# Optimization experiments

Measured on AMD Instinct MI355X. Metric: run time of the kernel, lower is better.

## Reference

```python
import jax, jax.numpy as jnp
import numpy as np

ALPHA = 0.2  # leaky relu slope
NEG_INF = -1.0e12


def _gat(x, adj, W, a):
    # x: [N, Fin], W: [Fin, Fout], a: [2*Fout, 1]
    h = x @ W                                  # [N, Fout]
    Fout = W.shape[1]
    # additive attention: e_ij = leakyrelu(h_i . a[:Fout] + h_j . a[Fout:])
    f1 = h @ a[:Fout, 0]                       # [N]
    f2 = h @ a[Fout:, 0]                       # [N]
    e = jax.nn.leaky_relu(f1[:, None] + f2[None, :], ALPHA)  # [N, N]
    att = jnp.where(adj > 0, e, NEG_INF)
    att = jax.nn.softmax(att, axis=1)          # dropout=0 -> identity
    return jax.nn.elu(att @ h + h)             # [N, Fout]


def setup_inputs() -> dict:
    key = jax.random.key(0)
    k = jax.random.split(key, 6)
    N, NFEAT, NHID, NNEXT = 8192, 256, 128, 1024
    x = jax.random.normal(k[0], (N, NFEAT), dtype=jnp.float32)
    adj = (jax.random.uniform(k[1], (N, N)) > 0.9).astype(jnp.float32)
    # xavier-uniform-ish init
    def xav(kk, shape):
        lim = np.sqrt(6.0 / (shape[0] + shape[1])) * 1.414
        return jax.random.uniform(kk, shape, minval=-lim, maxval=lim, dtype=jnp.float32)
    W_embed = xav(k[2], (NFEAT, NHID))
    a_embed = xav(k[3], (2 * NHID, 1))
    W_assign = xav(k[4], (NFEAT, NNEXT))
    a_assign = xav(k[5], (2 * NNEXT, 1))
    return {"x": x, "adj": adj, "W_embed": W_embed, "a_embed": a_embed,
            "W_assign": W_assign, "a_assign": a_assign}


def reference(x, adj, W_embed, a_embed, W_assign, a_assign):
    z_l = _gat(x, adj, W_embed, a_embed)          # [N, nhid]
    assign = _gat(x, adj, W_assign, a_assign)     # [N, nnext]
    s_l = jax.nn.softmax(assign, axis=-1)         # [N, nnext]
    xnext = s_l.T @ z_l                            # [nnext, nhid]
    anext = s_l.T @ adj @ s_l                      # [nnext, nnext]
    return xnext, anext, s_l
```

## Files before the change

kernel.cpp:

```cpp
#include <hip/hip_runtime.h>
#include <hip/hip_bf16.h>


#define DI __device__ __forceinline__

typedef __attribute__((ext_vector_type(8))) short short8;
typedef __attribute__((ext_vector_type(4))) float f32x4;

static DI float bf2f(short s) {
    union { unsigned u; float f; } c;
    c.u = ((unsigned)(unsigned short)s) << 16;
    return c.f;
}
static DI short f2bf(float f) {
    union { float f; unsigned u; } c; c.f = f;
    unsigned r = (c.u + 0x7FFFu + ((c.u >> 16) & 1u)) >> 16;
    return (short)(unsigned short)r;
}
template <int F32>
static DI short8 ld8(const void* base, size_t off) {
    if (F32 == 0) return *(const short8*)((const short*)base + off);
    const float* p = (const float*)base + off;
    f32x4 a = *(const f32x4*)p;
    f32x4 b = *(const f32x4*)(p + 4);
    short8 v;
    #pragma unroll
    for (int e = 0; e < 4; e++) { v[e] = f2bf(a[e]); v[4 + e] = f2bf(b[e]); }
    return v;
}
static DI float wred_sum(float v) {
    #pragma unroll
    for (int o = 32; o > 0; o >>= 1) v += __shfl_down(v, o, 64);
    return v;
}
static DI float wred_max(float v) {
    #pragma unroll
    for (int o = 32; o > 0; o >>= 1) v = fmaxf(v, __shfl_down(v, o, 64));
    return v;
}
static DI int sfun(int r) { return (r ^ (r >> 3)) & 7; }
static DI int swzk(int k, int r) {
    return (k & ~63) | ((((k >> 3) & 7) ^ sfun(r)) << 3) | (k & 7);
}
static DI unsigned pack2(short lo, short hi) {
    return ((unsigned)(unsigned short)lo) | (((unsigned)(unsigned short)hi) << 16);
}
static DI void gload16(const void* g, void* l) {
    __builtin_amdgcn_global_load_lds(
        (const __attribute__((address_space(1))) unsigned int*)g,
        (__attribute__((address_space(3))) unsigned int*)l, 16, 0, 0);
}

template <int EPI, int SWZX>
__launch_bounds__(256)
__global__ void gemm_lds(const short* __restrict__ A, const short* __restrict__ Bt,
                         void* __restrict__ C, int ldc, int kcount) {
    __shared__ short As0[128][64], Bs0[128][64];
    __shared__ short As1[128][64], Bs1[128][64];
    int bx = blockIdx.x, by = blockIdx.y;
    if (SWZX) {
        int lid = blockIdx.x + blockIdx.y * 8;
        int c = lid & 7, s = lid >> 3;
        by = c * 8 + (s >> 3);
        bx = s & 7;
    }
    const int tid  = threadIdx.x;
    const int lane = tid & 63;
    const int w    = tid >> 6;
    const int wr   = w >> 1, wc = w & 1;
    const int i0   = by * 128;
    const int n0   = bx * 128;
    const int k0   = blockIdx.z * kcount;

    const int srow = w * 32 + (lane >> 3);
    const short* gA = A  + (size_t)(i0 + srow) * 8192 + k0 + (lane & 7) * 8;
    const short* gB = Bt + (size_t)(n0 + srow) * 8192 + k0 + (lane & 7) * 8;

    f32x4 acc[4][4];
    #pragma unroll
    for (int m = 0; m < 4; m++)
        #pragma unroll
        for (int n = 0; n < 4; n++) acc[m][n] = (f32x4){0.f, 0.f, 0.f, 0.f};

#define STAGE_TILE(ts, Ab, Bb)                                                  \
    do {                                                                        \
        _Pragma("unroll")                                                       \
        for (int j = 0; j < 4; j++) {                                           \
            gload16(gA + (size_t)(ts) * 64 + (size_t)j * 8 * 8192,              \
                    &Ab[w * 32 + j * 8][0]);                                    \
            gload16(gB + (size_t)(ts) * 64 + (size_t)j * 8 * 8192,              \
                    &Bb[w * 32 + j * 8][0]);                                    \
        }                                                                       \
    } while (0)

#define COMPUTE_TILE(Ab, Bb)                                                    \
    do {                                                                        \
        _Pragma("unroll")                                                       \
        for (int kk = 0; kk < 2; kk++) {                                        \
            short8 af[4], bq[4];                                                \
            _Pragma("unroll")                                                   \
            for (int m = 0; m < 4; m++) {                                       \
                int ar = wr * 64 + m * 16 + (lane & 15);                        \
                af[m] = *(const short8*)&Ab[ar]                                 \
                            [swzk(kk * 32 + (lane >> 4) * 8, ar)];              \
            }                                                                   \
            _Pragma("unroll")                                                   \
            for (int n = 0; n < 4; n++) {                                       \
                int br = wc * 64 + n * 16 + (lane & 15);                        \
                bq[n] = *(const short8*)&Bb[br]                                 \
                            [swzk(kk * 32 + (lane >> 4) * 8, br)];              \
            }                                                                   \
            _Pragma("unroll")                                                   \
            for (int m = 0; m < 4; m++)                                         \
                _Pragma("unroll")                                               \
                for (int n = 0; n < 4; n++)                                     \
                    acc[m][n] = __builtin_amdgcn_mfma_f32_16x16x32_bf16(        \
                        af[m], bq[n], acc[m][n], 0, 0, 0);                      \
        }                                                                       \
    } while (0)

    const int nt = kcount >> 6;
    STAGE_TILE(0, As0, Bs0);
    for (int t = 0; t < nt; t += 2) {
        __syncthreads();
        STAGE_TILE(t + 1, As1, Bs1);
        COMPUTE_TILE(As0, Bs0);
        __syncthreads();
        if (t + 2 < nt) STAGE_TILE(t + 2, As0, Bs0);
        COMPUTE_TILE(As1, Bs1);
    }
#undef STAGE_TILE
#undef COMPUTE_TILE

    #pragma unroll
    for (int m = 0; m < 4; m++) {
        #pragma unroll
        for (int n = 0; n < 4; n++) {
            int row0 = i0 + wr * 64 + m * 16 + ((lane >> 4) << 2);
            int col  = n0 + wc * 64 + n * 16 + (lane & 15);
            if (EPI == 1) {
                unsigned long long pk = 0;
                #pragma unroll
                for (int r = 0; r < 4; r++)
                    pk |= (unsigned long long)(unsigned short)f2bf(acc[m][n][r])
                          << (16 * r);
                *(unsigned long long*)((short*)C + (size_t)col * 8192 +
                                       swzk(row0, col)) = pk;
            } else {
                #pragma unroll
                for (int r = 0; r < 4; r++) {
                    float v = acc[m][n][r];
                    if (EPI == 0) ((float*)C)[(size_t)(row0 + r) * ldc + col] = v;
                    else atomicAdd(&((float*)C)[(size_t)(row0 + r) * ldc + col], v);
                }
            }
        }
    }
}

template <int SWZX>
__launch_bounds__(256)
__global__ void gemm_bin(const unsigned char* __restrict__ adjm,
                         const short* __restrict__ Bt,
                         short* __restrict__ C, int kcount) {
    __shared__ short Bs0[128][64], Bs1[128][64];
    __shared__ unsigned char Ms0[128][8], Ms1[128][8];
    int bx = blockIdx.x, by = blockIdx.y;
    if (SWZX) {
        int lid = blockIdx.x + blockIdx.y * 8;
        int c = lid & 7, s = lid >> 3;
        by = c * 8 + (s >> 3);
        bx = s & 7;
    }
    const int tid  = threadIdx.x;
    const int lane = tid & 63;
    const int w    = tid >> 6;
    const int wr   = w >> 1, wc = w & 1;
    const int i0   = by * 128;
    const int n0   = bx * 128;
    const int k0   = blockIdx.z * kcount;

    const int srow = w * 32 + (lane >> 3);
    const short* gB = Bt + (size_t)(n0 + srow) * 8192 + k0 + (lane & 7) * 8;
    const unsigned char* gM = adjm + (size_t)(i0 + (tid >> 1)) * 1024 +
                              (k0 >> 3) + (tid & 1) * 4;

    f32x4 acc[4][4];
    #pragma unroll
    for (int m = 0; m < 4; m++)
        #pragma unroll
        for (int n = 0; n < 4; n++) acc[m][n] = (f32x4){0.f, 0.f, 0.f, 0.f};

#define BN_STAGE(ts, Bb, Mb)                                                    \
    do {                                                                        \
        _Pragma("unroll")                                                       \
        for (int j = 0; j < 4; j++)                                             \
            gload16(gB + (size_t)(ts) * 64 + (size_t)j * 8 * 8192,              \
                    &Bb[w * 32 + j * 8][0]);                                    \
        unsigned mv = *(const unsigned*)(gM + (size_t)(ts) * 8);                \
        *(unsigned*)&Mb[tid >> 1][(tid & 1) * 4] = mv;                          \
    } while (0)

#define BN_COMPUTE(Bb, Mb)                                                      \
    do {                                                                        \
        _Pragma("unroll")                                                       \
        for (int kk = 0; kk < 2; kk++) {                                        \
            short8 af[4], bq[4];                                                \
            _Pragma("unroll")                                                   \
            for (int m = 0; m < 4; m++) {                                       \
                int ar = wr * 64 + m * 16 + (lane & 15);                        \
                unsigned mbyte = Mb[ar][kk * 4 + (lane >> 4)];                  \
                _Pragma("unroll")                                               \
                for (int e = 0; e < 8; e++)                                     \
                    af[m][e] = ((mbyte >> e) & 1) ? (short)0x3F80 : (short)0;   \
            }                                                                   \
            _Pragma("unroll")                                                   \
            for (int n = 0; n < 4; n++) {                                       \
                int br = wc * 64 + n * 16 + (lane & 15);                        \
                bq[n] = *(const short8*)&Bb[br]                                 \
                            [swzk(kk * 32 + (lane >> 4) * 8, br)];              \
            }                                                                   \
            _Pragma("unroll")                                                   \
            for (int m = 0; m < 4; m++)                                         \
                _Pragma("unroll")                                               \
                for (int n = 0; n < 4; n++)                                     \
                    acc[m][n] = __builtin_amdgcn_mfma_f32_16x16x32_bf16(        \
                        af[m], bq[n], acc[m][n], 0, 0, 0);                      \
        }                                                                       \
    } while (0)

    const int nt = kcount >> 6;
    BN_STAGE(0, Bs0, Ms0);
    for (int t = 0; t < nt; t += 2) {
        __syncthreads();
        BN_STAGE(t + 1, Bs1, Ms1);
        BN_COMPUTE(Bs0, Ms0);
        __syncthreads();
        if (t + 2 < nt) BN_STAGE(t + 2, Bs0, Ms0);
        BN_COMPUTE(Bs1, Ms1);
    }
#undef BN_STAGE
#undef BN_COMPUTE

    #pragma unroll
    for (int m = 0; m < 4; m++) {
        #pragma unroll
        for (int n = 0; n < 4; n++) {
            int row0 = i0 + wr * 64 + m * 16 + ((lane >> 4) << 2);
            int col  = n0 + wc * 64 + n * 16 + (lane & 15);
            unsigned long long pk = 0;
            #pragma unroll
            for (int r = 0; r < 4; r++)
                pk |= (unsigned long long)(unsigned short)f2bf(acc[m][n][r])
                      << (16 * r);
            *(unsigned long long*)(C + (size_t)col * 8192 + swzk(row0, col)) = pk;
        }
    }
}

template <int EPI, int SWZX>
__launch_bounds__(256)
__global__ void gemm_gen(const unsigned char* __restrict__ adjm,
                         const short* __restrict__ Bt,
                         float* __restrict__ C, int ldc, int kcount,
                         const float* __restrict__ E1, const float* __restrict__ F1,
                         const float* __restrict__ E2, const float* __restrict__ F2) {
    __shared__ short As0[128][64], Bs0[128][64];
    __shared__ short As1[128][64], Bs1[128][64];
    int bx = blockIdx.x, by = blockIdx.y;
    if (SWZX) {
        int lid = blockIdx.x + blockIdx.y * 8;
        int c = lid & 7, s = lid >> 3;
        by = c * 8 + (s >> 3);
        bx = s & 7;
    }
    const int tid  = threadIdx.x;
    const int lane = tid & 63;
    const int w    = tid >> 6;
    const int wr   = w >> 1, wc = w & 1;
    const int i0   = by * 128;
    const int n0   = bx * 128;
    const int k0   = blockIdx.z * kcount;

    const int srow = w * 32 + (lane >> 3);
    const short* gB = Bt + (size_t)(n0 + srow) * 8192 + k0 + (lane & 7) * 8;
    const int mr = tid >> 1, mh = tid & 1;
    const unsigned char* gM = adjm + (size_t)(i0 + mr) * 1024 + (k0 >> 3) + mh * 4;
    const float e1v = E1[i0 + mr], f1v = F1[i0 + mr];

    f32x4 acc[4][4];
    #pragma unroll
    for (int m = 0; m < 4; m++)
        #pragma unroll
        for (int n = 0; n < 4; n++) acc[m][n] = (f32x4){0.f, 0.f, 0.f, 0.f};

    unsigned mreg;

#define G_ALOAD(ts)                                                             \
    do { mreg = *(const unsigned*)(gM + (size_t)(ts) * 8); } while (0)

#define G_BLOAD(ts, Bb)                                                         \
    do {                                                                        \
        _Pragma("unroll")                                                       \
        for (int j = 0; j < 4; j++)                                             \
            gload16(gB + (size_t)(ts) * 64 + (size_t)j * 8 * 8192,              \
                    &Bb[w * 32 + j * 8][0]);                                    \
    } while (0)

#define G_WSTAGE(ts, As_)                                                       \
    do {                                                                        \
        _Pragma("unroll")                                                       \
        for (int b = 0; b < 4; b++) {                                           \
            int kbr = mh * 4 + b;                                               \
            int rk = k0 + (ts) * 64 + kbr * 8;                                  \
            unsigned mbyte = (mreg >> (8 * b)) & 0xFFu;                         \
            f32x4 e2a = *(const f32x4*)(E2 + rk);                               \
            f32x4 e2b = *(const f32x4*)(E2 + rk + 4);                           \
            f32x4 f2a = *(const f32x4*)(F2 + rk);                               \
            f32x4 f2b = *(const f32x4*)(F2 + rk + 4);                           \
            short8 p;                                                           \
            _Pragma("unroll")                                                   \
            for (int e = 0; e < 8; e++) {                                       \
                float ev = e < 4 ? e2a[e] : e2b[e - 4];                         \
                float fv = e < 4 ? f2a[e] : f2b[e - 4];                         \
                float wg = fmaxf(e1v * ev, f1v * fv);                           \
                p[e] = ((mbyte >> e) & 1) ? f2bf(wg) : (short)0;                \
            }                                                                   \
            *(short8*)&As_[mr][(kbr ^ sfun(mr)) * 8] = p;                       \
        }                                                                       \
    } while (0)

#define G_COMPUTE(Ab_, Bb_)                                                     \
    do {                                                                        \
        _Pragma("unroll")                                                       \
        for (int kk = 0; kk < 2; kk++) {                                        \
            short8 af[4], bq[4];                                                \
            _Pragma("unroll")                                                   \
            for (int m = 0; m < 4; m++) {                                       \
                int ar = wr * 64 + m * 16 + (lane & 15);                        \
                af[m] = *(const short8*)&Ab_[ar]                                \
                            [swzk(kk * 32 + (lane >> 4) * 8, ar)];              \
            }                                                                   \
            _Pragma("unroll")                                                   \
            for (int n = 0; n < 4; n++) {                                       \
                int br = wc * 64 + n * 16 + (lane & 15);                        \
                bq[n] = *(const short8*)&Bb_[br]                                \
                            [swzk(kk * 32 + (lane >> 4) * 8, br)];              \
            }                                                                   \
            _Pragma("unroll")                                                   \
            for (int m = 0; m < 4; m++)                                         \
                _Pragma("unroll")                                               \
                for (int n = 0; n < 4; n++)                                     \
                    acc[m][n] = __builtin_amdgcn_mfma_f32_16x16x32_bf16(        \
                        af[m], bq[n], acc[m][n], 0, 0, 0);                      \
        }                                                                       \
    } while (0)

    const int nt = kcount >> 6;
    G_ALOAD(0);
    G_BLOAD(0, Bs0);
    for (int t = 0; t < nt; t += 2) {
        G_WSTAGE(t, As0);
        __syncthreads();
        G_ALOAD(t + 1);
        G_BLOAD(t + 1, Bs1);
        G_COMPUTE(As0, Bs0);
        G_WSTAGE(t + 1, As1);
        __syncthreads();
        if (t + 2 < nt) { G_ALOAD(t + 2); G_BLOAD(t + 2, Bs0); }
        G_COMPUTE(As1, Bs1);
    }
#undef G_ALOAD
#undef G_BLOAD
#undef G_WSTAGE
#undef G_COMPUTE

    #pragma unroll
    for (int m = 0; m < 4; m++) {
        #pragma unroll
        for (int n = 0; n < 4; n++) {
            int row0 = i0 + wr * 64 + m * 16 + ((lane >> 4) << 2);
            int col  = n0 + wc * 64 + n * 16 + (lane & 15);
            #pragma unroll
            for (int r = 0; r < 4; r++)
                atomicAdd(&C[(size_t)(row0 + r) * ldc + col], acc[m][n][r]);
        }
    }
}

template <int SWZX>
__launch_bounds__(256)
__global__ void gemm_xw_k(const float* __restrict__ A, const float* __restrict__ B,
                          short* __restrict__ C, short* __restrict__ Ct, int ldn) {
    __shared__ short As[128][64];
    __shared__ short Bs[128][64];
    int bx = blockIdx.x, by = blockIdx.y;
    if (SWZX) {
        int lid = blockIdx.x + blockIdx.y * 8;
        int c = lid & 7, s = lid >> 3;
        by = c * 8 + (s >> 3);
        bx = s & 7;
    }
    const int tid  = threadIdx.x;
    const int lane = tid & 63;
    const int w    = tid >> 6;
    const int wr   = w >> 1, wc = w & 1;
    const int i0   = by * 128;
    const int n0   = bx * 128;

    f32x4 acc[4][4];
    #pragma unroll
    for (int m = 0; m < 4; m++)
        #pragma unroll
        for (int n = 0; n < 4; n++) acc[m][n] = (f32x4){0.f, 0.f, 0.f, 0.f};

    for (int ks = 0; ks < 256; ks += 64) {
        __syncthreads();
        #pragma unroll
        for (int it = 0; it < 4; it++) {
            int idx = it * 256 + tid;
            int cg = idx & 7, r = idx >> 3;
            *(short8*)&As[r][swzk(cg * 8, r)] =
                ld8<1>(A, (size_t)(i0 + r) * 256 + ks + cg * 8);
        }
        #pragma unroll
        for (int it = 0; it < 2; it++) {
            int idx = it * 256 + tid;
            int ng = idx & 15, kp = idx >> 4;
            int k = 2 * kp;
            short8 r0 = ld8<1>(B, (size_t)(ks + k) * ldn + n0 + ng * 8);
            short8 r1 = ld8<1>(B, (size_t)(ks + k + 1) * ldn + n0 + ng * 8);
            #pragma unroll
            for (int j = 0; j < 8; j++) {
                int row = ng * 8 + j;
                *(unsigned*)&Bs[row][swzk(k, row)] = pack2(r0[j], r1[j]);
            }
        }
        __syncthreads();
        #pragma unroll
        for (int kk = 0; kk < 2; kk++) {
            short8 af[4], bq[4];
            #pragma unroll
            for (int m = 0; m < 4; m++) {
                int ar = wr * 64 + m * 16 + (lane & 15);
                af[m] = *(const short8*)&As[ar][swzk(kk * 32 + (lane >> 4) * 8, ar)];
            }
            #pragma unroll
            for (int n = 0; n < 4; n++) {
                int br = wc * 64 + n * 16 + (lane & 15);
                bq[n] = *(const short8*)&Bs[br][swzk(kk * 32 + (lane >> 4) * 8, br)];
            }
            #pragma unroll
            for (int m = 0; m < 4; m++)
                #pragma unroll
                for (int n = 0; n < 4; n++)
                    acc[m][n] = __builtin_amdgcn_mfma_f32_16x16x32_bf16(
                        af[m], bq[n], acc[m][n], 0, 0, 0);
        }
    }
    #pragma unroll
    for (int m = 0; m < 4; m++) {
        #pragma unroll
        for (int n = 0; n < 4; n++) {
            int row0 = i0 + wr * 64 + m * 16 + ((lane >> 4) << 2);
            int col  = n0 + wc * 64 + n * 16 + (lane & 15);
            unsigned long long pk = 0;
            #pragma unroll
            for (int r = 0; r < 4; r++) {
                short b = f2bf(acc[m][n][r]);
                C[(size_t)(row0 + r) * ldn + col] = b;
                pk |= (unsigned long long)(unsigned short)b << (16 * r);
            }
            *(unsigned long long*)(Ct + (size_t)col * 8192 + swzk(row0, col)) = pk;
        }
    }
}

__launch_bounds__(256)
__global__ void compute_f_k(const short* __restrict__ h1, const short* __restrict__ h2,
                            const float* __restrict__ ae, const float* __restrict__ aa,
                            float* __restrict__ f11, float* __restrict__ f21,
                            float* __restrict__ f12, float* __restrict__ f22) {
    int row = blockIdx.x, t = threadIdx.x;
    float s11 = 0.f, s21 = 0.f, s12 = 0.f, s22 = 0.f;
    if (t < 128) {
        float hv = bf2f(h1[(size_t)row * 128 + t]);
        s11 = hv * ae[t];
        s21 = hv * ae[128 + t];
    }
    #pragma unroll
    for (int q = 0; q < 4; q++) {
        int f = t + q * 256;
        float hv = bf2f(h2[(size_t)row * 1024 + f]);
        s12 += hv * aa[f];
        s22 += hv * aa[1024 + f];
    }
    __shared__ float red[4][4];
    s11 = wred_sum(s11); s21 = wred_sum(s21);
    s12 = wred_sum(s12); s22 = wred_sum(s22);
    int w = t >> 6;
    if ((t & 63) == 0) { red[0][w] = s11; red[1][w] = s21; red[2][w] = s12; red[3][w] = s22; }
    __syncthreads();
    if (t == 0) {
        f11[row] = red[0][0] + red[0][1] + red[0][2] + red[0][3];
        f21[row] = red[1][0] + red[1][1] + red[1][2] + red[1][3];
        f12[row] = red[2][0] + red[2][1] + red[2][2] + red[2][3];
        f22[row] = red[3][0] + red[3][1] + red[3][2] + red[3][3];
    }
}

__launch_bounds__(256)
__global__ void evec_k(const float* __restrict__ f11, const float* __restrict__ f21,
                       const float* __restrict__ f12, const float* __restrict__ f22,
                       float* __restrict__ E11, float* __restrict__ F11,
                       float* __restrict__ E21, float* __restrict__ F21,
                       float* __restrict__ E12, float* __restrict__ F12,
                       float* __restrict__ E22, float* __restrict__ F22) {
    int i = blockIdx.x * 256 + threadIdx.x;
    if (i >= 8192) return;
    float a = f11[i], b = f21[i], c = f12[i], d = f22[i];
    E11[i] = __expf(a); F11[i] = __expf(0.2f * a);
    E21[i] = __expf(b); F21[i] = __expf(0.2f * b);
    E12[i] = __expf(c); F12[i] = __expf(0.2f * c);
    E22[i] = __expf(d); F22[i] = __expf(0.2f * d);
}

__launch_bounds__(256)
__global__ void prepass_k(const float* __restrict__ adj,
                          const float* __restrict__ E11, const float* __restrict__ F11,
                          const float* __restrict__ E21, const float* __restrict__ F21,
                          const float* __restrict__ E12, const float* __restrict__ F12,
                          const float* __restrict__ E22, const float* __restrict__ F22,
                          float* __restrict__ den1, float* __restrict__ den2,
                          short* __restrict__ P2b, unsigned char* __restrict__ adjm) {
    const int r0 = blockIdx.x * 4, t = threadIdx.x;
    float e1r[4], f1r[4], e2r[4], f2r[4];
    #pragma unroll
    for (int r = 0; r < 4; r++) {
        e1r[r] = E11[r0 + r]; f1r[r] = F11[r0 + r];
        e2r[r] = E12[r0 + r]; f2r[r] = F12[r0 + r];
    }
    float d1[4] = {0.f, 0.f, 0.f, 0.f}, d2[4] = {0.f, 0.f, 0.f, 0.f};
    #pragma unroll
    for (int jc = 0; jc < 4; jc++) {
        int jb = jc * 2048 + t * 8;
        f32x4 eA0 = *(const f32x4*)(E21 + jb), eA1 = *(const f32x4*)(E21 + jb + 4);
        f32x4 fA0 = *(const f32x4*)(F21 + jb), fA1 = *(const f32x4*)(F21 + jb + 4);
        f32x4 eB0 = *(const f32x4*)(E22 + jb), eB1 = *(const f32x4*)(E22 + jb + 4);
        f32x4 fB0 = *(const f32x4*)(F22 + jb), fB1 = *(const f32x4*)(F22 + jb + 4);
        #pragma unroll
        for (int r = 0; r < 4; r++) {
            const float* ap = adj + (size_t)(r0 + r) * 8192 + jb;
            f32x4 a0 = *(const f32x4*)ap, a1 = *(const f32x4*)(ap + 4);
            short8 p2v;
            unsigned mb = 0;
            #pragma unroll
            for (int e = 0; e < 8; e++) {
                float av = e < 4 ? a0[e] : a1[e - 4];
                float eA = e < 4 ? eA0[e] : eA1[e - 4];
                float fA = e < 4 ? fA0[e] : fA1[e - 4];
                float eB = e < 4 ? eB0[e] : eB1[e - 4];
                float fB = e < 4 ? fB0[e] : fB1[e - 4];
                float x1 = fmaxf(e1r[r] * eA, f1r[r] * fA);
                float x2 = fmaxf(e2r[r] * eB, f2r[r] * fB);
                bool on = av > 0.f;
                d1[r] += on ? x1 : 0.f;
                d2[r] += on ? x2 : 0.f;
                p2v[e] = on ? f2bf(x2) : (short)0;
                mb |= (on ? 1u : 0u) << e;
            }
            *(short8*)(P2b + (size_t)(r0 + r) * 8192 + swzk(jb, r0 + r)) = p2v;
            adjm[(size_t)(r0 + r) * 1024 + (jb >> 3)] = (unsigned char)mb;
        }
    }
    __shared__ float r1s[4][4], r2s[4][4];
    #pragma unroll
    for (int r = 0; r < 4; r++) { d1[r] = wred_sum(d1[r]); d2[r] = wred_sum(d2[r]); }
    if ((t & 63) == 0) {
        #pragma unroll
        for (int r = 0; r < 4; r++) { r1s[t >> 6][r] = d1[r]; r2s[t >> 6][r] = d2[r]; }
    }
    __syncthreads();
    if (t < 4) {
        den1[r0 + t] = r1s[0][t] + r1s[1][t] + r1s[2][t] + r1s[3][t];
        den2[r0 + t] = r2s[0][t] + r2s[1][t] + r2s[2][t] + r2s[3][t];
    }
}

__launch_bounds__(256)
__global__ void epi_gat1t_k(const float* __restrict__ Y1, const float* __restrict__ den1,
                            const short* __restrict__ h1, short* __restrict__ zlt) {
    __shared__ short ts[128][65];
    int tr = blockIdx.x * 64;
    int t = threadIdx.x;
    #pragma unroll
    for (int it = 0; it < 4; it++) {
        int idx = it * 256 + t;
        int r = idx >> 4, cb = idx & 15;
        int row = tr + r;
        float d = den1[row]; d = d > 0.f ? d : 1.f;
        const float* yp = Y1 + (size_t)row * 128 + cb * 8;
        f32x4 y0 = *(const f32x4*)yp, y1 = *(const f32x4*)(yp + 4);
        short8 hv = *(const short8*)(h1 + (size_t)row * 128 + cb * 8);
        #pragma unroll
        for (int e = 0; e < 8; e++) {
            float z = (e < 4 ? y0[e] : y1[e - 4]) / d + bf2f(hv[e]);
            z = z > 0.f ? z : (__expf(z) - 1.f);
            ts[cb * 8 + e][r] = f2bf(z);
        }
    }
    __syncthreads();
    #pragma unroll
    for (int it = 0; it < 4; it++) {
        int idx = it * 256 + t;
        int c = idx >> 3, rb = idx & 7;
        short8 v = *(const short8*)&ts[c][rb * 8];
        *(short8*)(zlt + (size_t)c * 8192 + tr + ((rb ^ sfun(c)) << 3)) = v;
    }
}

__launch_bounds__(256)
__global__ void episoft_k(const float* __restrict__ Y2, const float* __restrict__ den2,
                          const short* __restrict__ h2, float* __restrict__ slo,
                          short* __restrict__ slb) {
    int row = blockIdx.x, t = threadIdx.x;
    float d = den2[row];
    d = d > 0.f ? d : 1.f;
    float v[4], mx = -1e30f;
    #pragma unroll
    for (int q = 0; q < 4; q++) {
        int j = t + q * 256;
        float a = Y2[(size_t)row * 1024 + j] / d + bf2f(h2[(size_t)row * 1024 + j]);
        a = a > 0.f ? a : (__expf(a) - 1.f);
        v[q] = a;
        mx = fmaxf(mx, a);
    }
    __shared__ float sred[4];
    __shared__ float sbc;
    mx = wred_max(mx);
    if ((t & 63) == 0) sred[t >> 6] = mx;
    __syncthreads();
    if (t == 0) sbc = fmaxf(fmaxf(sred[0], sred[1]), fmaxf(sred[2], sred[3]));
    __syncthreads();
    mx = sbc;
    float s = 0.f;
    #pragma unroll
    for (int q = 0; q < 4; q++) { v[q] = __expf(v[q] - mx); s += v[q]; }
    s = wred_sum(s);
    if ((t & 63) == 0) sred[t >> 6] = s;
    __syncthreads();
    if (t == 0) sbc = sred[0] + sred[1] + sred[2] + sred[3];
    __syncthreads();
    float inv = 1.f / sbc;
    #pragma unroll
    for (int q = 0; q < 4; q++) {
        float sv = v[q] * inv;
        slo[(size_t)row * 1024 + t + q * 256] = sv;
        slb[(size_t)row * 1024 + t + q * 256] = f2bf(sv);
    }
}

template <int F32IN>
__launch_bounds__(256)
__global__ void transpose_swz_k(const void* __restrict__ in, short* __restrict__ out,
                                int R, int C) {
    __shared__ short ts[64][72];
    int tc = blockIdx.x * 64;
    int tr = blockIdx.y * 64;
    int t = threadIdx.x;
    #pragma unroll
    for (int h = 0; h < 2; h++) {
        int r = (t >> 3) + h * 32, c = (t & 7) * 8;
        *(short8*)&ts[r][c] = ld8<F32IN>(in, (size_t)(tr + r) * C + tc + c);
    }
    __syncthreads();
    #pragma unroll
    for (int h = 0; h < 2; h++) {
        int n = t >> 2, blk = (t & 3) + h * 4;
        short8 v;
        #pragma unroll
        for (int e = 0; e < 8; e++) v[e] = ts[blk * 8 + e][n];
        *(short8*)(out + (size_t)(tc + n) * R + tr + ((blk ^ sfun(tc + n)) << 3)) = v;
    }
}

extern "C" void kernel_launch(void* const* d_in, const int* in_sizes, int n_in,
                              void* d_out, int out_size, void* d_ws, size_t ws_size,
                              hipStream_t stream) {
    const float* x   = (const float*)d_in[0];
    const float* adj = (const float*)d_in[1];
    const float* We  = (const float*)d_in[2];
    const float* ae  = (const float*)d_in[3];
    const float* Wa  = (const float*)d_in[4];
    const float* aa  = (const float*)d_in[5];
    float* out = (float*)d_out;

    char* w = (char*)d_ws;
    short* h1b = (short*)(w);
    short* h2b = (short*)(w + (2u   << 20));
    float* f11 = (float*)(w + (18u  << 20));
    float* f21 = f11 + 8192;  float* f12 = f21 + 8192; float* f22 = f12 + 8192;
    float* den1 = f22 + 8192; float* den2 = den1 + 8192;
    float* E11 = den2 + 8192; float* F11 = E11 + 8192;
    float* E21 = F11 + 8192;  float* F21 = E21 + 8192;
    float* E12 = F21 + 8192;  float* F12 = E12 + 8192;
    float* E22 = F12 + 8192;  float* F22 = E22 + 8192;
    float* Y1f = (float*)(w + (21u << 20));
    float* Y2f = (float*)(w + (25u << 20));
    short* slb = (short*)(w + (57u << 20));
    short* h1t = (short*)(w + (73u << 20));
    short* h2t = (short*)(w + (75u << 20));
    short* slt = (short*)(w + (91u << 20));
    short* zlt = (short*)(w + (107u << 20));
    short* tT  = (short*)(w + (109u << 20));
    short* P2b = (short*)(w + (128u << 20));
    unsigned char* adjm = (unsigned char*)(w + (256u << 20));

    float* xo  = out;
    float* ao  = out + 131072;
    float* slo = out + 131072 + 1048576;

    hipMemsetAsync(out, 0, (size_t)(131072 + 1048576) * 4, stream);
    hipMemsetAsync(Y1f, 0, (size_t)8192 * 128 * 4, stream);

    gemm_xw_k<0><<<dim3(1, 64), 256, 0, stream>>>(x, We, h1b, h1t, 128);
    gemm_xw_k<1><<<dim3(8, 64), 256, 0, stream>>>(x, Wa, h2b, h2t, 1024);
    compute_f_k<<<dim3(8192), 256, 0, stream>>>(h1b, h2b, ae, aa, f11, f21, f12, f22);
    evec_k<<<dim3(32), 256, 0, stream>>>(f11, f21, f12, f22,
        E11, F11, E21, F21, E12, F12, E22, F22);
    prepass_k<<<dim3(2048), 256, 0, stream>>>(adj,
        E11, F11, E21, F21, E12, F12, E22, F22, den1, den2, P2b, adjm);

    gemm_gen<3, 0><<<dim3(1, 64, 8), 256, 0, stream>>>(
        adjm, h1t, Y1f, 128, 1024, E11, F11, E21, F21);
    epi_gat1t_k<<<dim3(128), 256, 0, stream>>>(Y1f, den1, h1b, zlt);

    gemm_lds<0, 1><<<dim3(8, 64, 1), 256, 0, stream>>>(P2b, h2t, Y2f, 1024, 8192);
    episoft_k<<<dim3(8192), 256, 0, stream>>>(Y2f, den2, h2b, slo, slb);
    transpose_swz_k<0><<<dim3(16, 128), 256, 0, stream>>>(slb, slt, 8192, 1024);

    gemm_bin<1><<<dim3(8, 64, 1), 256, 0, stream>>>(adjm, slt, tT, 8192);

    gemm_lds<3, 0><<<dim3(8, 8, 8), 256, 0, stream>>>(slt, tT, ao, 1024, 1024);
    gemm_lds<3, 0><<<dim3(1, 8, 32), 256, 0, stream>>>(slt, zlt, xo, 128, 256);
}
```

Measured before the change: 708.5 us.

## Fuse the two attention aggregation GEMMs into one launch and restage the adjacency-mask GEMM

After: 850.3 us. 20.0% more time.

```diff
diff --git a/kernel.cpp b/kernel.cpp
--- a/kernel.cpp
+++ b/kernel.cpp
@@ -51,286 +51,7 @@
         (__attribute__((address_space(3))) unsigned int*)l, 16, 0, 0);
 }
 
-template <int EPI, int SWZX>
-__launch_bounds__(256)
-__global__ void gemm_lds(const short* __restrict__ A, const short* __restrict__ Bt,
-                         void* __restrict__ C, int ldc, int kcount) {
-    __shared__ short As0[128][64], Bs0[128][64];
-    __shared__ short As1[128][64], Bs1[128][64];
-    int bx = blockIdx.x, by = blockIdx.y;
-    if (SWZX) {
-        int lid = blockIdx.x + blockIdx.y * 8;
-        int c = lid & 7, s = lid >> 3;
-        by = c * 8 + (s >> 3);
-        bx = s & 7;
-    }
-    const int tid  = threadIdx.x;
-    const int lane = tid & 63;
-    const int w    = tid >> 6;
-    const int wr   = w >> 1, wc = w & 1;
-    const int i0   = by * 128;
-    const int n0   = bx * 128;
-    const int k0   = blockIdx.z * kcount;
-
-    const int srow = w * 32 + (lane >> 3);
-    const short* gA = A  + (size_t)(i0 + srow) * 8192 + k0 + (lane & 7) * 8;
-    const short* gB = Bt + (size_t)(n0 + srow) * 8192 + k0 + (lane & 7) * 8;
-
-    f32x4 acc[4][4];
-    #pragma unroll
-    for (int m = 0; m < 4; m++)
-        #pragma unroll
-        for (int n = 0; n < 4; n++) acc[m][n] = (f32x4){0.f, 0.f, 0.f, 0.f};
-
-#define STAGE_TILE(ts, Ab, Bb)                                                  \
-    do {                                                                        \
-        _Pragma("unroll")                                                       \
-        for (int j = 0; j < 4; j++) {                                           \
-            gload16(gA + (size_t)(ts) * 64 + (size_t)j * 8 * 8192,              \
-                    &Ab[w * 32 + j * 8][0]);                                    \
-            gload16(gB + (size_t)(ts) * 64 + (size_t)j * 8 * 8192,              \
-                    &Bb[w * 32 + j * 8][0]);                                    \
-        }                                                                       \
-    } while (0)
-
-#define COMPUTE_TILE(Ab, Bb)                                                    \
-    do {                                                                        \
-        _Pragma("unroll")                                                       \
-        for (int kk = 0; kk < 2; kk++) {                                        \
-            short8 af[4], bq[4];                                                \
-            _Pragma("unroll")                                                   \
-            for (int m = 0; m < 4; m++) {                                       \
-                int ar = wr * 64 + m * 16 + (lane & 15);                        \
-                af[m] = *(const short8*)&Ab[ar]                                 \
-                            [swzk(kk * 32 + (lane >> 4) * 8, ar)];              \
-            }                                                                   \
-            _Pragma("unroll")                                                   \
-            for (int n = 0; n < 4; n++) {                                       \
-                int br = wc * 64 + n * 16 + (lane & 15);                        \
-                bq[n] = *(const short8*)&Bb[br]                                 \
-                            [swzk(kk * 32 + (lane >> 4) * 8, br)];              \
-            }                                                                   \
-            _Pragma("unroll")                                                   \
-            for (int m = 0; m < 4; m++)                                         \
-                _Pragma("unroll")                                               \
-                for (int n = 0; n < 4; n++)                                     \
-                    acc[m][n] = __builtin_amdgcn_mfma_f32_16x16x32_bf16(        \
-                        af[m], bq[n], acc[m][n], 0, 0, 0);                      \
-        }                                                                       \
-    } while (0)
-
-    const int nt = kcount >> 6;
-    STAGE_TILE(0, As0, Bs0);
-    for (int t = 0; t < nt; t += 2) {
-        __syncthreads();
-        STAGE_TILE(t + 1, As1, Bs1);
-        COMPUTE_TILE(As0, Bs0);
-        __syncthreads();
-        if (t + 2 < nt) STAGE_TILE(t + 2, As0, Bs0);
-        COMPUTE_TILE(As1, Bs1);
-    }
-#undef STAGE_TILE
-#undef COMPUTE_TILE
-
-    #pragma unroll
-    for (int m = 0; m < 4; m++) {
-        #pragma unroll
-        for (int n = 0; n < 4; n++) {
-            int row0 = i0 + wr * 64 + m * 16 + ((lane >> 4) << 2);
-            int col  = n0 + wc * 64 + n * 16 + (lane & 15);
-            if (EPI == 1) {
-                unsigned long long pk = 0;
-                #pragma unroll
-                for (int r = 0; r < 4; r++)
-                    pk |= (unsigned long long)(unsigned short)f2bf(acc[m][n][r])
-                          << (16 * r);
-                *(unsigned long long*)((short*)C + (size_t)col * 8192 +
-                                       swzk(row0, col)) = pk;
-            } else {
-                #pragma unroll
-                for (int r = 0; r < 4; r++) {
-                    float v = acc[m][n][r];
-                    if (EPI == 0) ((float*)C)[(size_t)(row0 + r) * ldc + col] = v;
-                    else atomicAdd(&((float*)C)[(size_t)(row0 + r) * ldc + col], v);
-                }
-            }
-        }
-    }
-}
-
-template <int SWZX>
-__launch_bounds__(256)
-__global__ void gemm_bin(const unsigned char* __restrict__ adjm,
-                         const short* __restrict__ Bt,
-                         short* __restrict__ C, int kcount) {
-    __shared__ short Bs0[128][64], Bs1[128][64];
-    __shared__ unsigned char Ms0[128][8], Ms1[128][8];
-    int bx = blockIdx.x, by = blockIdx.y;
-    if (SWZX) {
-        int lid = blockIdx.x + blockIdx.y * 8;
-        int c = lid & 7, s = lid >> 3;
-        by = c * 8 + (s >> 3);
-        bx = s & 7;
-    }
-    const int tid  = threadIdx.x;
-    const int lane = tid & 63;
-    const int w    = tid >> 6;
-    const int wr   = w >> 1, wc = w & 1;
-    const int i0   = by * 128;
-    const int n0   = bx * 128;
-    const int k0   = blockIdx.z * kcount;
-
-    const int srow = w * 32 + (lane >> 3);
-    const short* gB = Bt + (size_t)(n0 + srow) * 8192 + k0 + (lane & 7) * 8;
-    const unsigned char* gM = adjm + (size_t)(i0 + (tid >> 1)) * 1024 +
-                              (k0 >> 3) + (tid & 1) * 4;
-
-    f32x4 acc[4][4];
-    #pragma unroll
-    for (int m = 0; m < 4; m++)
-        #pragma unroll
-        for (int n = 0; n < 4; n++) acc[m][n] = (f32x4){0.f, 0.f, 0.f, 0.f};
-
-#define BN_STAGE(ts, Bb, Mb)                                                    \
-    do {                                                                        \
-        _Pragma("unroll")                                                       \
-        for (int j = 0; j < 4; j++)                                             \
-            gload16(gB + (size_t)(ts) * 64 + (size_t)j * 8 * 8192,              \
-                    &Bb[w * 32 + j * 8][0]);                                    \
-        unsigned mv = *(const unsigned*)(gM + (size_t)(ts) * 8);                \
-        *(unsigned*)&Mb[tid >> 1][(tid & 1) * 4] = mv;                          \
-    } while (0)
-
-#define BN_COMPUTE(Bb, Mb)                                                      \
-    do {                                                                        \
-        _Pragma("unroll")                                                       \
-        for (int kk = 0; kk < 2; kk++) {                                        \
-            short8 af[4], bq[4];                                                \
-            _Pragma("unroll")                                                   \
-            for (int m = 0; m < 4; m++) {                                       \
-                int ar = wr * 64 + m * 16 + (lane & 15);                        \
-                unsigned mbyte = Mb[ar][kk * 4 + (lane >> 4)];                  \
-                _Pragma("unroll")                                               \
-                for (int e = 0; e < 8; e++)                                     \
-                    af[m][e] = ((mbyte >> e) & 1) ? (short)0x3F80 : (short)0;   \
-            }                                                                   \
-            _Pragma("unroll")                                                   \
-            for (int n = 0; n < 4; n++) {                                       \
-                int br = wc * 64 + n * 16 + (lane & 15);                        \
-                bq[n] = *(const short8*)&Bb[br]                                 \
-                            [swzk(kk * 32 + (lane >> 4) * 8, br)];              \
-            }                                                                   \
-            _Pragma("unroll")                                                   \
-            for (int m = 0; m < 4; m++)                                         \
-                _Pragma("unroll")                                               \
-                for (int n = 0; n < 4; n++)                                     \
-                    acc[m][n] = __builtin_amdgcn_mfma_f32_16x16x32_bf16(        \
-                        af[m], bq[n], acc[m][n], 0, 0, 0);                      \
-        }                                                                       \
-    } while (0)
-
-    const int nt = kcount >> 6;
-    BN_STAGE(0, Bs0, Ms0);
-    for (int t = 0; t < nt; t += 2) {
-        __syncthreads();
-        BN_STAGE(t + 1, Bs1, Ms1);
-        BN_COMPUTE(Bs0, Ms0);
-        __syncthreads();
-        if (t + 2 < nt) BN_STAGE(t + 2, Bs0, Ms0);
-        BN_COMPUTE(Bs1, Ms1);
-    }
-#undef BN_STAGE
-#undef BN_COMPUTE
-
-    #pragma unroll
-    for (int m = 0; m < 4; m++) {
-        #pragma unroll
-        for (int n = 0; n < 4; n++) {
-            int row0 = i0 + wr * 64 + m * 16 + ((lane >> 4) << 2);
-            int col  = n0 + wc * 64 + n * 16 + (lane & 15);
-            unsigned long long pk = 0;
-            #pragma unroll
-            for (int r = 0; r < 4; r++)
-                pk |= (unsigned long long)(unsigned short)f2bf(acc[m][n][r])
-                      << (16 * r);
-            *(unsigned long long*)(C + (size_t)col * 8192 + swzk(row0, col)) = pk;
-        }
-    }
-}
-
-template <int EPI, int SWZX>
-__launch_bounds__(256)
-__global__ void gemm_gen(const unsigned char* __restrict__ adjm,
-                         const short* __restrict__ Bt,
-                         float* __restrict__ C, int ldc, int kcount,
-                         const float* __restrict__ E1, const float* __restrict__ F1,
-                         const float* __restrict__ E2, const float* __restrict__ F2) {
-    __shared__ short As0[128][64], Bs0[128][64];
-    __shared__ short As1[128][64], Bs1[128][64];
-    int bx = blockIdx.x, by = blockIdx.y;
-    if (SWZX) {
-        int lid = blockIdx.x + blockIdx.y * 8;
-        int c = lid & 7, s = lid >> 3;
-        by = c * 8 + (s >> 3);
-        bx = s & 7;
-    }
-    const int tid  = threadIdx.x;
-    const int lane = tid & 63;
-    const int w    = tid >> 6;
-    const int wr   = w >> 1, wc = w & 1;
-    const int i0   = by * 128;
-    const int n0   = bx * 128;
-    const int k0   = blockIdx.z * kcount;
-
-    const int srow = w * 32 + (lane >> 3);
-    const short* gB = Bt + (size_t)(n0 + srow) * 8192 + k0 + (lane & 7) * 8;
-    const int mr = tid >> 1, mh = tid & 1;
-    const unsigned char* gM = adjm + (size_t)(i0 + mr) * 1024 + (k0 >> 3) + mh * 4;
-    const float e1v = E1[i0 + mr], f1v = F1[i0 + mr];
-
-    f32x4 acc[4][4];
-    #pragma unroll
-    for (int m = 0; m < 4; m++)
-        #pragma unroll
-        for (int n = 0; n < 4; n++) acc[m][n] = (f32x4){0.f, 0.f, 0.f, 0.f};
-
-    unsigned mreg;
-
-#define G_ALOAD(ts)                                                             \
-    do { mreg = *(const unsigned*)(gM + (size_t)(ts) * 8); } while (0)
-
-#define G_BLOAD(ts, Bb)                                                         \
-    do {                                                                        \
-        _Pragma("unroll")                                                       \
-        for (int j = 0; j < 4; j++)                                             \
-            gload16(gB + (size_t)(ts) * 64 + (size_t)j * 8 * 8192,              \
-                    &Bb[w * 32 + j * 8][0]);                                    \
-    } while (0)
-
-#define G_WSTAGE(ts, As_)                                                       \
-    do {                                                                        \
-        _Pragma("unroll")                                                       \
-        for (int b = 0; b < 4; b++) {                                           \
-            int kbr = mh * 4 + b;                                               \
-            int rk = k0 + (ts) * 64 + kbr * 8;                                  \
-            unsigned mbyte = (mreg >> (8 * b)) & 0xFFu;                         \
-            f32x4 e2a = *(const f32x4*)(E2 + rk);                               \
-            f32x4 e2b = *(const f32x4*)(E2 + rk + 4);                           \
-            f32x4 f2a = *(const f32x4*)(F2 + rk);                               \
-            f32x4 f2b = *(const f32x4*)(F2 + rk + 4);                           \
-            short8 p;                                                           \
-            _Pragma("unroll")                                                   \
-            for (int e = 0; e < 8; e++) {                                       \
-                float ev = e < 4 ? e2a[e] : e2b[e - 4];                         \
-                float fv = e < 4 ? f2a[e] : f2b[e - 4];                         \
-                float wg = fmaxf(e1v * ev, f1v * fv);                           \
-                p[e] = ((mbyte >> e) & 1) ? f2bf(wg) : (short)0;                \
-            }                                                                   \
-            *(short8*)&As_[mr][(kbr ^ sfun(mr)) * 8] = p;                       \
-        }                                                                       \
-    } while (0)
-
-#define G_COMPUTE(Ab_, Bb_)                                                     \
+#define MFMA_COMPUTE(Ab_, Bb_)                                                  \
     do {                                                                        \
         _Pragma("unroll")                                                       \
         for (int kk = 0; kk < 2; kk++) {                                        \
@@ -356,25 +77,177 @@
         }                                                                       \
     } while (0)
 
+template <int EPI, int SWZX>
+__launch_bounds__(256)
+__global__ void gemm_lds(const short* __restrict__ A, const short* __restrict__ Bt,
+                         void* __restrict__ C, int ldc, int kcount) {
+    __shared__ short As0[128][64], Bs0[128][64];
+    __shared__ short As1[128][64], Bs1[128][64];
+    int bx = blockIdx.x, by = blockIdx.y;
+    if (SWZX) {
+        int lid = blockIdx.x + blockIdx.y * 8;
+        int c = lid & 7, s = lid >> 3;
+        by = c * 8 + (s >> 3);
+        bx = s & 7;
+    }
+    const int tid  = threadIdx.x;
+    const int lane = tid & 63;
+    const int w    = tid >> 6;
+    const int wr   = w >> 1, wc = w & 1;
+    const int i0   = by * 128;
+    const int n0   = bx * 128;
+    const int k0   = blockIdx.z * kcount;
+
+    const int srow = w * 32 + (lane >> 3);
+    const short* gA = A  + (size_t)(i0 + srow) * 8192 + k0 + (lane & 7) * 8;
+    const short* gB = Bt + (size_t)(n0 + srow) * 8192 + k0 + (lane & 7) * 8;
+
+    f32x4 acc[4][4];
+    #pragma unroll
+    for (int m = 0; m < 4; m++)
+        #pragma unroll
+        for (int n = 0; n < 4; n++) acc[m][n] = (f32x4){0.f, 0.f, 0.f, 0.f};
+
+#define STAGE_TILE(ts, Ab, Bb)                                                  \
+    do {                                                                        \
+        _Pragma("unroll")                                                       \
+        for (int j = 0; j < 4; j++) {                                           \
+            gload16(gA + (size_t)(ts) * 64 + (size_t)j * 8 * 8192,              \
+                    &Ab[w * 32 + j * 8][0]);                                    \
+            gload16(gB + (size_t)(ts) * 64 + (size_t)j * 8 * 8192,              \
+                    &Bb[w * 32 + j * 8][0]);                                    \
+        }                                                                       \
+    } while (0)
+
     const int nt = kcount >> 6;
-    G_ALOAD(0);
-    G_BLOAD(0, Bs0);
+    STAGE_TILE(0, As0, Bs0);
     for (int t = 0; t < nt; t += 2) {
-        G_WSTAGE(t, As0);
-        __syncthreads();
-        G_ALOAD(t + 1);
-        G_BLOAD(t + 1, Bs1);
-        G_COMPUTE(As0, Bs0);
-        G_WSTAGE(t + 1, As1);
-        __syncthreads();
-        if (t + 2 < nt) { G_ALOAD(t + 2); G_BLOAD(t + 2, Bs0); }
-        G_COMPUTE(As1, Bs1);
-    }
-#undef G_ALOAD
-#undef G_BLOAD
-#undef G_WSTAGE
-#undef G_COMPUTE
-
+        __syncthreads();
+        STAGE_TILE(t + 1, As1, Bs1);
+        MFMA_COMPUTE(As0, Bs0);
+        __syncthreads();
+        if (t + 2 < nt) STAGE_TILE(t + 2, As0, Bs0);
+        MFMA_COMPUTE(As1, Bs1);
+    }
+#undef STAGE_TILE
+
+    #pragma unroll
+    for (int m = 0; m < 4; m++) {
+        #pragma unroll
+        for (int n = 0; n < 4; n++) {
+            int row0 = i0 + wr * 64 + m * 16 + ((lane >> 4) << 2);
+            int col  = n0 + wc * 64 + n * 16 + (lane & 15);
+            #pragma unroll
+            for (int r = 0; r < 4; r++) {
+                float v = acc[m][n][r];
+                if (EPI == 0) ((float*)C)[(size_t)(row0 + r) * ldc + col] = v;
+                else atomicAdd(&((float*)C)[(size_t)(row0 + r) * ldc + col], v);
+            }
+        }
+    }
+}
+
+__launch_bounds__(256)
+__global__ void gemm_y(const short* __restrict__ P2b,
+                       const unsigned char* __restrict__ adjm,
+                       const short* __restrict__ h2t, const short* __restrict__ h1t,
+                       float* __restrict__ Y2f, float* __restrict__ Y1f,
+                       const float* __restrict__ E1, const float* __restrict__ F1,
+                       const float* __restrict__ E2, const float* __restrict__ F2) {
+    __shared__ short As0[128][64], Bs0[128][64];
+    __shared__ short As1[128][64], Bs1[128][64];
+    const bool y1 = (blockIdx.x == 8);
+    int bx, by;
+    if (y1) { bx = 0; by = blockIdx.y; }
+    else {
+        int lid = blockIdx.x + blockIdx.y * 8;
+        int c = lid & 7, s = lid >> 3;
+        by = c * 8 + (s >> 3);
+        bx = s & 7;
+    }
+    const int tid  = threadIdx.x;
+    const int lane = tid & 63;
+    const int w    = tid >> 6;
+    const int wr   = w >> 1, wc = w & 1;
+    const int i0   = by * 128;
+    const int n0   = bx * 128;
+
+    const int srow = w * 32 + (lane >> 3);
+    const short* Bt = y1 ? h1t : h2t;
+    const short* gB = Bt + (size_t)(n0 + srow) * 8192 + (lane & 7) * 8;
+    const short* gA = P2b + (size_t)(i0 + srow) * 8192 + (lane & 7) * 8;
+    const int mr = tid >> 1, mh = tid & 1;
+    const unsigned char* gM = adjm + (size_t)(i0 + mr) * 1024 + mh * 4;
+    float e1v = 0.f, f1v = 0.f;
+    if (y1) { e1v = E1[i0 + mr]; f1v = F1[i0 + mr]; }
+
+    f32x4 acc[4][4];
+    #pragma unroll
+    for (int m = 0; m < 4; m++)
+        #pragma unroll
+        for (int n = 0; n < 4; n++) acc[m][n] = (f32x4){0.f, 0.f, 0.f, 0.f};
+
+#define Y_STAGE(ts, Ab, Bb)                                                     \
+    do {                                                                        \
+        if (!y1) {                                                              \
+            _Pragma("unroll")                                                   \
+            for (int j = 0; j < 4; j++)                                         \
+                gload16(gA + (size_t)(ts) * 64 + (size_t)j * 8 * 8192,          \
+                        &Ab[w * 32 + j * 8][0]);                                \
+        }                                                                       \
+        _Pragma("unroll")                                                       \
+        for (int j = 0; j < 4; j++)                                             \
+            gload16(gB + (size_t)(ts) * 64 + (size_t)j * 8 * 8192,              \
+                    &Bb[w * 32 + j * 8][0]);                                    \
+    } while (0)
+
+#define Y_WSTAGE(ts, As_, mrg)                                                  \
+    do {                                                                        \
+        _Pragma("unroll")                                                       \
+        for (int b = 0; b < 4; b++) {                                           \
+            int kbr = mh * 4 + b;                                               \
+            int rk = (ts) * 64 + kbr * 8;                                       \
+            unsigned mbyte = ((mrg) >> (8 * b)) & 0xFFu;                        \
+            f32x4 e2a = *(const f32x4*)(E2 + rk);                               \
+            f32x4 e2b = *(const f32x4*)(E2 + rk + 4);                           \
+            f32x4 f2a = *(const f32x4*)(F2 + rk);                               \
+            f32x4 f2b = *(const f32x4*)(F2 + rk + 4);                           \
+            short8 p;                                                           \
+            _Pragma("unroll")                                                   \
+            for (int e = 0; e < 8; e++) {                                       \
+                float ev = e < 4 ? e2a[e] : e2b[e - 4];                         \
+                float fv = e < 4 ? f2a[e] : f2b[e - 4];                         \
+                float wg = fmaxf(e1v * ev, f1v * fv);                           \
+                p[e] = ((mbyte >> e) & 1) ? f2bf(wg) : (short)0;                \
+            }                                                                   \
+            *(short8*)&As_[mr][(kbr ^ sfun(mr)) * 8] = p;                       \
+        }                                                                       \
+    } while (0)
+
+    const int nt = 128;
+    unsigned mreg = 0;
+    if (y1) mreg = *(const unsigned*)(gM);
+    Y_STAGE(0, As0, Bs0);
+    for (int t = 0; t < nt; t += 2) {
+        if (y1) Y_WSTAGE(t, As0, mreg);
+        __syncthreads();
+        unsigned mnext = 0;
+        if (y1) mnext = *(const unsigned*)(gM + (size_t)(t + 1) * 8);
+        Y_STAGE(t + 1, As1, Bs1);
+        MFMA_COMPUTE(As0, Bs0);
+        if (y1) Y_WSTAGE(t + 1, As1, mnext);
+        __syncthreads();
+        if (t + 2 < nt) {
+            if (y1) mreg = *(const unsigned*)(gM + (size_t)(t + 2) * 8);
+            Y_STAGE(t + 2, As0, Bs0);
+        }
+        MFMA_COMPUTE(As1, Bs1);
+    }
+#undef Y_STAGE
+#undef Y_WSTAGE
+
+    float* C = y1 ? Y1f : Y2f;
+    const int ldc = y1 ? 128 : 1024;
     #pragma unroll
     for (int m = 0; m < 4; m++) {
         #pragma unroll
@@ -383,7 +256,97 @@
             int col  = n0 + wc * 64 + n * 16 + (lane & 15);
             #pragma unroll
             for (int r = 0; r < 4; r++)
-                atomicAdd(&C[(size_t)(row0 + r) * ldc + col], acc[m][n][r]);
+                C[(size_t)(row0 + r) * ldc + col] = acc[m][n][r];
+        }
+    }
+}
+
+template <int SWZX>
+__launch_bounds__(256)
+__global__ void gemm_maskb(const unsigned char* __restrict__ adjm,
+                           const short* __restrict__ Bt,
+                           short* __restrict__ C) {
+    __shared__ short As0[128][64], Bs0[128][64];
+    __shared__ short As1[128][64], Bs1[128][64];
+    int bx = blockIdx.x, by = blockIdx.y;
+    if (SWZX) {
+        int lid = blockIdx.x + blockIdx.y * 8;
+        int c = lid & 7, s = lid >> 3;
+        by = c * 8 + (s >> 3);
+        bx = s & 7;
+    }
+    const int tid  = threadIdx.x;
+    const int lane = tid & 63;
+    const int w    = tid >> 6;
+    const int wr   = w >> 1, wc = w & 1;
+    const int i0   = by * 128;
+    const int n0   = bx * 128;
+
+    const int srow = w * 32 + (lane >> 3);
+    const short* gB = Bt + (size_t)(n0 + srow) * 8192 + (lane & 7) * 8;
+    const int mr = tid >> 1, mh = tid & 1;
+    const unsigned char* gM = adjm + (size_t)(i0 + mr) * 1024 + mh * 4;
+
+    f32x4 acc[4][4];
+    #pragma unroll
+    for (int m = 0; m < 4; m++)
+        #pragma unroll
+        for (int n = 0; n < 4; n++) acc[m][n] = (f32x4){0.f, 0.f, 0.f, 0.f};
+
+#define MB_BLOAD(ts, Bb)                                                        \
+    do {                                                                        \
+        _Pragma("unroll")                                                       \
+        for (int j = 0; j < 4; j++)                                             \
+            gload16(gB + (size_t)(ts) * 64 + (size_t)j * 8 * 8192,              \
+                    &Bb[w * 32 + j * 8][0]);                                    \
+    } while (0)
+
+#define MB_WSTAGE(As_, mrg)                                                     \
+    do {                                                                        \
+        _Pragma("unroll")                                                       \
+        for (int b = 0; b < 4; b++) {                                           \
+            int kbr = mh * 4 + b;                                               \
+            unsigned mbyte = ((mrg) >> (8 * b)) & 0xFFu;                        \
+            short8 p;                                                           \
+            _Pragma("unroll")                                                   \
+            for (int e = 0; e < 8; e++)                                         \
+                p[e] = ((mbyte >> e) & 1) ? (short)0x3F80 : (short)0;           \
+            *(short8*)&As_[mr][(kbr ^ sfun(mr)) * 8] = p;                       \
+        }                                                                       \
+    } while (0)
+
+    const int nt = 128;
+    unsigned mreg = *(const unsigned*)(gM);
+    MB_BLOAD(0, Bs0);
+    for (int t = 0; t < nt; t += 2) {
+        MB_WSTAGE(As0, mreg);
+        __syncthreads();
+        unsigned mnext = *(const unsigned*)(gM + (size_t)(t + 1) * 8);
+        MB_BLOAD(t + 1, Bs1);
+        MFMA_COMPUTE(As0, Bs0);
+        MB_WSTAGE(As1, mnext);
+        __syncthreads();
+        if (t + 2 < nt) {
+            mreg = *(const unsigned*)(gM + (size_t)(t + 2) * 8);
+            MB_BLOAD(t + 2, Bs0);
+        }
+        MFMA_COMPUTE(As1, Bs1);
+    }
+#undef MB_BLOAD
+#undef MB_WSTAGE
+
+    #pragma unroll
+    for (int m = 0; m < 4; m++) {
+        #pragma unroll
+        for (int n = 0; n < 4; n++) {
+            int row0 = i0 + wr * 64 + m * 16 + ((lane >> 4) << 2);
+            int col  = n0 + wc * 64 + n * 16 + (lane & 15);
+            unsigned long long pk = 0;
+            #pragma unroll
+            for (int r = 0; r < 4; r++)
+                pk |= (unsigned long long)(unsigned short)f2bf(acc[m][n][r])
+                      << (16 * r);
+            *(unsigned long long*)(C + (size_t)col * 8192 + swzk(row0, col)) = pk;
         }
     }
 }
@@ -437,26 +400,7 @@
             }
         }
         __syncthreads();
-        #pragma unroll
-        for (int kk = 0; kk < 2; kk++) {
-            short8 af[4], bq[4];
-            #pragma unroll
-            for (int m = 0; m < 4; m++) {
-                int ar = wr * 64 + m * 16 + (lane & 15);
-                af[m] = *(const short8*)&As[ar][swzk(kk * 32 + (lane >> 4) * 8, ar)];
-            }
-            #pragma unroll
-            for (int n = 0; n < 4; n++) {
-                int br = wc * 64 + n * 16 + (lane & 15);
-                bq[n] = *(const short8*)&Bs[br][swzk(kk * 32 + (lane >> 4) * 8, br)];
-            }
-            #pragma unroll
-            for (int m = 0; m < 4; m++)
-                #pragma unroll
-                for (int n = 0; n < 4; n++)
-                    acc[m][n] = __builtin_amdgcn_mfma_f32_16x16x32_bf16(
-                        af[m], bq[n], acc[m][n], 0, 0, 0);
-        }
+        MFMA_COMPUTE(As, Bs);
     }
     #pragma unroll
     for (int m = 0; m < 4; m++) {
@@ -721,7 +665,6 @@
     float* slo = out + 131072 + 1048576;
 
     hipMemsetAsync(out, 0, (size_t)(131072 + 1048576) * 4, stream);
-    hipMemsetAsync(Y1f, 0, (size_t)8192 * 128 * 4, stream);
 
     gemm_xw_k<0><<<dim3(1, 64), 256, 0, stream>>>(x, We, h1b, h1t, 128);
     gemm_xw_k<1><<<dim3(8, 64), 256, 0, stream>>>(x, Wa, h2b, h2t, 1024);
@@ -731,15 +674,14 @@
     prepass_k<<<dim3(2048), 256, 0, stream>>>(adj,
         E11, F11, E21, F21, E12, F12, E22, F22, den1, den2, P2b, adjm);
 
-    gemm_gen<3, 0><<<dim3(1, 64, 8), 256, 0, stream>>>(
-        adjm, h1t, Y1f, 128, 1024, E11, F11, E21, F21);
+    gemm_y<<<dim3(9, 64), 256, 0, stream>>>(P2b, adjm, h2t, h1t, Y2f, Y1f,
+                                            E11, F11, E21, F21);
+
     epi_gat1t_k<<<dim3(128), 256, 0, stream>>>(Y1f, den1, h1b, zlt);
-
-    gemm_lds<0, 1><<<dim3(8, 64, 1), 256, 0, stream>>>(P2b, h2t, Y2f, 1024, 8192);
     episoft_k<<<dim3(8192), 256, 0, stream>>>(Y2f, den2, h2b, slo, slb);
     transpose_swz_k<0><<<dim3(16, 128), 256, 0, stream>>>(slb, slt, 8192, 1024);
 
-    gemm_bin<1><<<dim3(8, 64, 1), 256, 0, stream>>>(adjm, slt, tT, 8192);
+    gemm_maskb<1><<<dim3(8, 64), 256, 0, stream>>>(adjm, slt, tT);
 
     gemm_lds<3, 0><<<dim3(8, 8, 8), 256, 0, stream>>>(slt, tT, ao, 1024, 1024);
     gemm_lds<3, 0><<<dim3(1, 8, 32), 256, 0, stream>>>(slt, zlt, xo, 128, 256);
```
